# Kernel optimization log

Hardware: AMD Instinct MI355X
Metric: run time of the kernel (lower is better)

## Reference

```python
import jax, jax.numpy as jnp
import numpy as np

BN_EPS = 1e-5


def setup_inputs() -> dict:
    key = jax.random.key(0)
    ks = jax.random.split(key, 8)
    B, T, D, Tu, Dout, M = 32, 4096, 128, 512, 64, 8
    feats = jax.random.normal(ks[0], (B, T, D), dtype=jnp.float32)
    # integer time-window ids stored in channel 0 of x; pin 0 and Tu-1 so
    # tw_uniq = arange(0, Tu) exactly (no -99 padding) for every batch row
    tw = jax.random.randint(ks[1], (B, T), 0, Tu)
    tw = tw.at[:, 0].set(0).at[:, 1].set(Tu - 1)
    x = jnp.concatenate([tw[..., None].astype(jnp.float32), feats], axis=-1)
    mask = jax.random.uniform(ks[2], (B, T, 1)) < 0.9
    mask = mask.at[:, :2].set(True)  # keep pinned min/max entries valid
    tw_uniq = jnp.broadcast_to(jnp.arange(Tu, dtype=jnp.float32)[None, :, None], (B, Tu, 1))
    bn_gamma = jax.random.uniform(ks[3], (D,), jnp.float32, 0.5, 1.5)
    bn_beta = 0.1 * jax.random.normal(ks[4], (D,), dtype=jnp.float32)
    bn_mean = jnp.zeros((D,), jnp.float32)
    bn_var = jnp.ones((D,), jnp.float32)
    conv_w = jax.random.normal(ks[5], (Dout, D), dtype=jnp.float32) / np.float32(np.sqrt(D))
    conv_b = jnp.zeros((Dout,), jnp.float32)
    fc_w = jax.random.normal(ks[6], (M, Dout), dtype=jnp.float32) / np.float32(np.sqrt(Dout))
    fc_b = jnp.zeros((M,), jnp.float32)
    return dict(x=x, mask=mask, tw_uniq=tw_uniq, bn_gamma=bn_gamma, bn_beta=bn_beta,
                bn_mean=bn_mean, bn_var=bn_var, conv_w=conv_w, conv_b=conv_b,
                fc_w=fc_w, fc_b=fc_b)


def reference(x, mask, tw_uniq, bn_gamma, bn_beta, bn_mean, bn_var,
              conv_w, conv_b, fc_w, fc_b):
    # --- TimeWindowPooling (segment-max form of the dense expand+where+amax) ---
    # torch computes amax_T(where(tw==tw_uniq & mask, x, 0)) -> max(0, group max).
    # Equivalent: scatter-max of mask-zeroed values into a zeros-initialized
    # (B, Tu, D) buffer, avoiding the O(B*T*Tu*D) blowup.
    tw = x[..., 0]           # (B, T) integer-valued, detached in torch
    feats = x[..., 1:]       # (B, T, D)
    B, T, D = feats.shape
    Tu = tw_uniq.shape[1]
    u0 = tw_uniq[:, 0, 0]    # per-batch window minimum
    idx = jnp.clip((tw - u0[:, None]).astype(jnp.int32), 0, Tu - 1)  # (B, T)
    vals = jnp.where(mask, feats, 0.0)  # masked rows contribute 0 == init value
    hidden = jnp.zeros((B, Tu, D), feats.dtype).at[jnp.arange(B)[:, None], idx].max(vals)
    # --- mlp_down: BatchNorm1d (inference stats) + 1x1 Conv1d over channels ---
    h = (hidden - bn_mean) * jax.lax.rsqrt(bn_var + BN_EPS) * bn_gamma + bn_beta
    h = jnp.einsum('bud,od->buo', h, conv_w) + conv_b  # (B, Tu, Dout)
    # --- fc_out ---
    return jnp.einsum('buo,mo->bum', h, fc_w) + fc_b   # (B, Tu, M)
```

## Files before the change

### kernel.cpp

```cpp
#include <hip/hip_runtime.h>

#define B_   32
#define T_   4096
#define D_   128
#define TU   512
#define M_   8
#define O_   64
#define CAP  64
#define BN_EPS 1e-5f

typedef float f4u __attribute__((ext_vector_type(4), aligned(4)));

#define WS_CNT 0
#define WS_ROW (B_ * TU)


__global__ __launch_bounds__(512) void fill_kernel(
    const float* __restrict__ x, const int* __restrict__ mask,
    const float* __restrict__ tw_uniq, int* __restrict__ wsI) {
    const int g = blockIdx.x * 512 + threadIdx.x;
    const int b = g >> 12;
    const int t = g & (T_ - 1);
    const float twf = x[(size_t)g * (D_ + 1)];
    if (mask[g] == 0) return;
    const float u0 = tw_uniq[b * TU];
    const int   u  = min(max((int)(twf - u0), 0), TU - 1);
    const int  bin = b * TU + u;
    const int  pos = atomicAdd(&wsI[WS_CNT + bin], 1);
    if (pos < CAP) wsI[WS_ROW + bin * CAP + pos] = t;
}

__global__ __launch_bounds__(1024, 8) void gather_mm_kernel(
    const float* __restrict__ x,
    const float* __restrict__ bn_gamma, const float* __restrict__ bn_beta,
    const float* __restrict__ bn_mean,  const float* __restrict__ bn_var,
    const float* __restrict__ conv_w,   const float* __restrict__ conv_b,
    const float* __restrict__ fc_w,     const float* __restrict__ fc_b,
    const int* __restrict__ wsI, float* __restrict__ out) {
    __shared__ float wsm[M_ * D_];
    __shared__ float tmp[M_ * D_];
    __shared__ float biasc[M_];
    const int j = blockIdx.x;
    const int b  = (j & 7) + 8 * ((j >> 3) & 3);
    const int uc = j >> 5;
    const int tid = threadIdx.x;

    {
        const int m = tid >> 7, d = tid & (D_ - 1);
        float wraw = 0.f;
        for (int o = 0; o < O_; ++o) wraw += fc_w[m * O_ + o] * conv_w[o * D_ + d];
        const float sc = bn_gamma[d] * rsqrtf(bn_var[d] + BN_EPS);
        const float sh = bn_beta[d] - bn_mean[d] * sc;
        wsm[tid] = wraw * sc;
        tmp[tid] = wraw * sh;
    }
    __syncthreads();
    if (tid < M_) {
        float s = fc_b[tid];
        for (int o = 0; o < O_; ++o) s += fc_w[tid * O_ + o] * conv_b[o];
        for (int d = 0; d < D_; ++d) s += tmp[tid * D_ + d];
        biasc[tid] = s;
    }
    __syncthreads();

    const int w    = tid >> 6;
    const int lane = tid & 63;
    const int half = lane >> 5;
    const int lq   = lane & 31;
    const float* xb = x + (size_t)b * T_ * (D_ + 1);

    const int u      = uc * 32 + w * 2 + half;
    const int bin    = b * TU + u;
    const int n      = min(wsI[WS_CNT + bin], CAP);
    const int* rowbin = wsI + WS_ROW + (size_t)bin * CAP;
    const int nn     = min(n, 32);
    int myidx = 0;
    if (lq < nn) myidx = rowbin[lq];

    float a0 = 0.f, a1 = 0.f, a2 = 0.f, a3 = 0.f;
#define ROWP(i) (const f4u*)(xb + (size_t)__shfl(myidx, (half << 5) + (i)) * (D_ + 1) + 1 + (lq << 2))
    for (int bs = 0; bs < nn; bs += 8) {
        const int m = nn - bs;
        f4u t0, t1, t2, t3, t4, t5, t6, t7;
        if (m > 0) t0 = *ROWP(bs + 0);
        if (m > 1) t1 = *ROWP(bs + 1);
        if (m > 2) t2 = *ROWP(bs + 2);
        if (m > 3) t3 = *ROWP(bs + 3);
        if (m > 4) t4 = *ROWP(bs + 4);
        if (m > 5) t5 = *ROWP(bs + 5);
        if (m > 6) t6 = *ROWP(bs + 6);
        if (m > 7) t7 = *ROWP(bs + 7);
        if (m > 0) { a0 = fmaxf(a0, t0.x); a1 = fmaxf(a1, t0.y); a2 = fmaxf(a2, t0.z); a3 = fmaxf(a3, t0.w); }
        if (m > 1) { a0 = fmaxf(a0, t1.x); a1 = fmaxf(a1, t1.y); a2 = fmaxf(a2, t1.z); a3 = fmaxf(a3, t1.w); }
        if (m > 2) { a0 = fmaxf(a0, t2.x); a1 = fmaxf(a1, t2.y); a2 = fmaxf(a2, t2.z); a3 = fmaxf(a3, t2.w); }
        if (m > 3) { a0 = fmaxf(a0, t3.x); a1 = fmaxf(a1, t3.y); a2 = fmaxf(a2, t3.z); a3 = fmaxf(a3, t3.w); }
        if (m > 4) { a0 = fmaxf(a0, t4.x); a1 = fmaxf(a1, t4.y); a2 = fmaxf(a2, t4.z); a3 = fmaxf(a3, t4.w); }
        if (m > 5) { a0 = fmaxf(a0, t5.x); a1 = fmaxf(a1, t5.y); a2 = fmaxf(a2, t5.z); a3 = fmaxf(a3, t5.w); }
        if (m > 6) { a0 = fmaxf(a0, t6.x); a1 = fmaxf(a1, t6.y); a2 = fmaxf(a2, t6.z); a3 = fmaxf(a3, t6.w); }
        if (m > 7) { a0 = fmaxf(a0, t7.x); a1 = fmaxf(a1, t7.y); a2 = fmaxf(a2, t7.z); a3 = fmaxf(a3, t7.w); }
    }
#undef ROWP
    for (int i2 = 32; i2 < n; ++i2) {
        const f4u v = *(const f4u*)(xb + (size_t)rowbin[i2] * (D_ + 1) + 1 + (lq << 2));
        a0 = fmaxf(a0, v.x); a1 = fmaxf(a1, v.y);
        a2 = fmaxf(a2, v.z); a3 = fmaxf(a3, v.w);
    }

    const int db = lq << 2;
    float p0, p1, p2, p3, p4, p5, p6, p7;
#define PDOT(mm) (a0 * wsm[(mm) * D_ + db] + a1 * wsm[(mm) * D_ + db + 1] + \
                  a2 * wsm[(mm) * D_ + db + 2] + a3 * wsm[(mm) * D_ + db + 3])
    p0 = PDOT(0); p1 = PDOT(1); p2 = PDOT(2); p3 = PDOT(3);
    p4 = PDOT(4); p5 = PDOT(5); p6 = PDOT(6); p7 = PDOT(7);
#undef PDOT
#pragma unroll
    for (int off = 1; off < 32; off <<= 1) {
        p0 += __shfl_xor(p0, off); p1 += __shfl_xor(p1, off);
        p2 += __shfl_xor(p2, off); p3 += __shfl_xor(p3, off);
        p4 += __shfl_xor(p4, off); p5 += __shfl_xor(p5, off);
        p6 += __shfl_xor(p6, off); p7 += __shfl_xor(p7, off);
    }
    if (lq == 0) {
        float* op = out + ((size_t)(b * TU + u)) * M_;
        *(float4*)(op)     = make_float4(p0 + biasc[0], p1 + biasc[1],
                                         p2 + biasc[2], p3 + biasc[3]);
        *(float4*)(op + 4) = make_float4(p4 + biasc[4], p5 + biasc[5],
                                         p6 + biasc[6], p7 + biasc[7]);
    }
}

extern "C" void kernel_launch(void* const* d_in, const int* in_sizes, int n_in,
                              void* d_out, int out_size, void* d_ws, size_t ws_size,
                              hipStream_t stream) {
    const float* x        = (const float*)d_in[0];
    const int*   mask     = (const int*)  d_in[1];
    const float* tw_uniq  = (const float*)d_in[2];
    const float* bn_gamma = (const float*)d_in[3];
    const float* bn_beta  = (const float*)d_in[4];
    const float* bn_mean  = (const float*)d_in[5];
    const float* bn_var   = (const float*)d_in[6];
    const float* conv_w   = (const float*)d_in[7];
    const float* conv_b   = (const float*)d_in[8];
    const float* fc_w     = (const float*)d_in[9];
    const float* fc_b     = (const float*)d_in[10];
    int*   wsI = (int*)d_ws;
    float* out = (float*)d_out;

    hipMemsetAsync(wsI, 0, B_ * TU * sizeof(int), stream);
    fill_kernel<<<256, 512, 0, stream>>>(x, mask, tw_uniq, wsI);
    gather_mm_kernel<<<512, 1024, 0, stream>>>(
        x, bn_gamma, bn_beta, bn_mean, bn_var,
        conv_w, conv_b, fc_w, fc_b, wsI, out);
}
```

Measured before the change: 130.4 us.

## Replace bin-list gather with LDS atomic-max scatter tiles and merge pass

Replaces the two-pass bin-index build plus random row gather with a scatter kernel. Each block streams a contiguous quarter of the time axis for one batch and one 64-channel half, and scatter-maxes the positive values into a zeroed LDS tile using unsigned-int atomicMax with XOR swizzling. Partial tiles go to workspace, and the second kernel max-merges the four partials before the folded BN/conv/fc dot products. This swaps random, uncoalesced gathers and the memset for coalesced streaming reads, at the cost of LDS atomic contention and 128 KB of LDS per block, which limits occupancy.

```diff
diff --git a/kernel.cpp b/kernel.cpp
--- a/kernel.cpp
+++ b/kernel.cpp
@@ -6,37 +6,82 @@
 #define TU   512
 #define M_   8
 #define O_   64
-#define CAP  64
+#define HW   64
+#define TILE (TU * HW)
+#define TSL  1024
 #define BN_EPS 1e-5f
 
 typedef float f4u __attribute__((ext_vector_type(4), aligned(4)));
 
-#define WS_CNT 0
-#define WS_ROW (B_ * TU)
 
 
-__global__ __launch_bounds__(512) void fill_kernel(
-    const float* __restrict__ x, const int* __restrict__ mask,
-    const float* __restrict__ tw_uniq, int* __restrict__ wsI) {
-    const int g = blockIdx.x * 512 + threadIdx.x;
-    const int b = g >> 12;
-    const int t = g & (T_ - 1);
-    const float twf = x[(size_t)g * (D_ + 1)];
-    if (mask[g] == 0) return;
-    const float u0 = tw_uniq[b * TU];
-    const int   u  = min(max((int)(twf - u0), 0), TU - 1);
-    const int  bin = b * TU + u;
-    const int  pos = atomicAdd(&wsI[WS_CNT + bin], 1);
-    if (pos < CAP) wsI[WS_ROW + bin * CAP + pos] = t;
+__global__ __launch_bounds__(1024) void scatter_kernel(
+    const float* __restrict__ x,
+    const int*   __restrict__ mask,
+    const float* __restrict__ tw_uniq,
+    float*       __restrict__ wsF) {
+    __shared__ unsigned hid[TILE];
+    __shared__ int uidxs[TSL];
+    const int i = blockIdx.x;
+    const int b = (i & 7) + 8 * ((i >> 3) & 3);
+    const int r = i >> 5;
+    const int h = r >> 2;
+    const int q = r & 3;
+    const int tid = threadIdx.x;
+    const int tb = q * TSL;
+
+    const float* xb = x + (size_t)b * T_ * (D_ + 1);
+
+    const float twf = xb[(size_t)(tb + tid) * (D_ + 1)];
+    const int   mk  = mask[b * T_ + tb + tid];
+    const float u0  = tw_uniq[b * TU];
+
+#pragma unroll
+    for (int c = 0; c < TILE / 4096; ++c)
+        *(float4*)&hid[c * 4096 + tid * 4] = make_float4(0.f, 0.f, 0.f, 0.f);
+
+    uidxs[tid] = mk ? min(max((int)(twf - u0), 0), TU - 1) : -1;
+    __syncthreads();
+
+    const int rloc = tid >> 4;
+    const int lq   = tid & 15;
+    const float* fb = xb + 1 + h * HW + lq * 4;
+    for (int it = 0; it < TSL / 64 / 8; ++it) {
+        f4u fv[8];
+        int uu[8];
+#pragma unroll
+        for (int j = 0; j < 8; ++j) {
+            const int t = tb + (it * 8 + j) * 64 + rloc;
+            fv[j] = *(const f4u*)(fb + (size_t)t * (D_ + 1));
+        }
+#pragma unroll
+        for (int j = 0; j < 8; ++j)
+            uu[j] = uidxs[(it * 8 + j) * 64 + rloc];
+#pragma unroll
+        for (int j = 0; j < 8; ++j) {
+            if (uu[j] >= 0) {
+                unsigned* hp = &hid[(uu[j] << 6) + ((lq ^ (uu[j] & 15)) << 2)];
+                if (fv[j].x > 0.f) atomicMax(hp + 0, __float_as_uint(fv[j].x));
+                if (fv[j].y > 0.f) atomicMax(hp + 1, __float_as_uint(fv[j].y));
+                if (fv[j].z > 0.f) atomicMax(hp + 2, __float_as_uint(fv[j].z));
+                if (fv[j].w > 0.f) atomicMax(hp + 3, __float_as_uint(fv[j].w));
+            }
+        }
+    }
+    __syncthreads();
+
+    float* tp = wsF + (size_t)(((b * 2 + h) << 2) + q) * TILE;
+#pragma unroll
+    for (int c = 0; c < TILE / 4096; ++c)
+        *(float4*)(tp + c * 4096 + tid * 4) = *(const float4*)&hid[c * 4096 + tid * 4];
 }
 
-__global__ __launch_bounds__(1024, 8) void gather_mm_kernel(
-    const float* __restrict__ x,
+__global__ __launch_bounds__(1024) void merge_mm_kernel(
     const float* __restrict__ bn_gamma, const float* __restrict__ bn_beta,
     const float* __restrict__ bn_mean,  const float* __restrict__ bn_var,
     const float* __restrict__ conv_w,   const float* __restrict__ conv_b,
     const float* __restrict__ fc_w,     const float* __restrict__ fc_b,
-    const int* __restrict__ wsI, float* __restrict__ out) {
+    const float* __restrict__ wsF, float* __restrict__ out) {
     __shared__ float wsm[M_ * D_];
     __shared__ float tmp[M_ * D_];
     __shared__ float biasc[M_];
@@ -66,47 +111,23 @@
     const int w    = tid >> 6;
     const int lane = tid & 63;
     const int half = lane >> 5;
-    const int lq   = lane & 31;
-    const float* xb = x + (size_t)b * T_ * (D_ + 1);
+    const int l5   = lane & 31;
+    const int u    = uc * 32 + w * 2 + half;
+    const int hh   = l5 >> 4;
+    const int dq   = l5 & 15;
+    const int slot = dq ^ (u & 15);
 
-    const int u      = uc * 32 + w * 2 + half;
-    const int bin    = b * TU + u;
-    const int n      = min(wsI[WS_CNT + bin], CAP);
-    const int* rowbin = wsI + WS_ROW + (size_t)bin * CAP;
-    const int nn     = min(n, 32);
-    int myidx = 0;
-    if (lq < nn) myidx = rowbin[lq];
+    const float* tp = wsF + (size_t)((b * 2 + hh) << 2) * TILE + u * HW + slot * 4;
+    const float4 v0 = *(const float4*)(tp);
+    const float4 v1 = *(const float4*)(tp + TILE);
+    const float4 v2 = *(const float4*)(tp + 2 * TILE);
+    const float4 v3 = *(const float4*)(tp + 3 * TILE);
+    const float a0 = fmaxf(fmaxf(v0.x, v1.x), fmaxf(v2.x, v3.x));
+    const float a1 = fmaxf(fmaxf(v0.y, v1.y), fmaxf(v2.y, v3.y));
+    const float a2 = fmaxf(fmaxf(v0.z, v1.z), fmaxf(v2.z, v3.z));
+    const float a3 = fmaxf(fmaxf(v0.w, v1.w), fmaxf(v2.w, v3.w));
 
-    float a0 = 0.f, a1 = 0.f, a2 = 0.f, a3 = 0.f;
-#define ROWP(i) (const f4u*)(xb + (size_t)__shfl(myidx, (half << 5) + (i)) * (D_ + 1) + 1 + (lq << 2))
-    for (int bs = 0; bs < nn; bs += 8) {
-        const int m = nn - bs;
-        f4u t0, t1, t2, t3, t4, t5, t6, t7;
-        if (m > 0) t0 = *ROWP(bs + 0);
-        if (m > 1) t1 = *ROWP(bs + 1);
-        if (m > 2) t2 = *ROWP(bs + 2);
-        if (m > 3) t3 = *ROWP(bs + 3);
-        if (m > 4) t4 = *ROWP(bs + 4);
-        if (m > 5) t5 = *ROWP(bs + 5);
-        if (m > 6) t6 = *ROWP(bs + 6);
-        if (m > 7) t7 = *ROWP(bs + 7);
-        if (m > 0) { a0 = fmaxf(a0, t0.x); a1 = fmaxf(a1, t0.y); a2 = fmaxf(a2, t0.z); a3 = fmaxf(a3, t0.w); }
-        if (m > 1) { a0 = fmaxf(a0, t1.x); a1 = fmaxf(a1, t1.y); a2 = fmaxf(a2, t1.z); a3 = fmaxf(a3, t1.w); }
-        if (m > 2) { a0 = fmaxf(a0, t2.x); a1 = fmaxf(a1, t2.y); a2 = fmaxf(a2, t2.z); a3 = fmaxf(a3, t2.w); }
-        if (m > 3) { a0 = fmaxf(a0, t3.x); a1 = fmaxf(a1, t3.y); a2 = fmaxf(a2, t3.z); a3 = fmaxf(a3, t3.w); }
-        if (m > 4) { a0 = fmaxf(a0, t4.x); a1 = fmaxf(a1, t4.y); a2 = fmaxf(a2, t4.z); a3 = fmaxf(a3, t4.w); }
-        if (m > 5) { a0 = fmaxf(a0, t5.x); a1 = fmaxf(a1, t5.y); a2 = fmaxf(a2, t5.z); a3 = fmaxf(a3, t5.w); }
-        if (m > 6) { a0 = fmaxf(a0, t6.x); a1 = fmaxf(a1, t6.y); a2 = fmaxf(a2, t6.z); a3 = fmaxf(a3, t6.w); }
-        if (m > 7) { a0 = fmaxf(a0, t7.x); a1 = fmaxf(a1, t7.y); a2 = fmaxf(a2, t7.z); a3 = fmaxf(a3, t7.w); }
-    }
-#undef ROWP
-    for (int i2 = 32; i2 < n; ++i2) {
-        const f4u v = *(const f4u*)(xb + (size_t)rowbin[i2] * (D_ + 1) + 1 + (lq << 2));
-        a0 = fmaxf(a0, v.x); a1 = fmaxf(a1, v.y);
-        a2 = fmaxf(a2, v.z); a3 = fmaxf(a3, v.w);
-    }
-
-    const int db = lq << 2;
+    const int db = l5 << 2;
     float p0, p1, p2, p3, p4, p5, p6, p7;
 #define PDOT(mm) (a0 * wsm[(mm) * D_ + db] + a1 * wsm[(mm) * D_ + db + 1] + \
                   a2 * wsm[(mm) * D_ + db + 2] + a3 * wsm[(mm) * D_ + db + 3])
@@ -120,7 +141,7 @@
         p4 += __shfl_xor(p4, off); p5 += __shfl_xor(p5, off);
         p6 += __shfl_xor(p6, off); p7 += __shfl_xor(p7, off);
     }
-    if (lq == 0) {
+    if (l5 == 0) {
         float* op = out + ((size_t)(b * TU + u)) * M_;
         *(float4*)(op)     = make_float4(p0 + biasc[0], p1 + biasc[1],
                                          p2 + biasc[2], p3 + biasc[3]);
@@ -143,12 +164,11 @@
     const float* conv_b   = (const float*)d_in[8];
     const float* fc_w     = (const float*)d_in[9];
     const float* fc_b     = (const float*)d_in[10];
-    int*   wsI = (int*)d_ws;
+    float* wsF = (float*)d_ws;
     float* out = (float*)d_out;
 
-    hipMemsetAsync(wsI, 0, B_ * TU * sizeof(int), stream);
-    fill_kernel<<<256, 512, 0, stream>>>(x, mask, tw_uniq, wsI);
-    gather_mm_kernel<<<512, 1024, 0, stream>>>(
-        x, bn_gamma, bn_beta, bn_mean, bn_var,
-        conv_w, conv_b, fc_w, fc_b, wsI, out);
+    scatter_kernel<<<256, 1024, 0, stream>>>(x, mask, tw_uniq, wsF);
+    merge_mm_kernel<<<512, 1024, 0, stream>>>(
+        bn_gamma, bn_beta, bn_mean, bn_var,
+        conv_w, conv_b, fc_w, fc_b, wsF, out);
 }
```

New measurement: 136.4 us. 4.6% more time.
